# Kernel tuning notes

Hardware: AMD Instinct MI355X
Metric: run time of the kernel (lower is better)

Reference implementation:

```python
import jax, jax.numpy as jnp
import numpy as np

NT = ['SB', 'PQ', 'PV', 'NB']
SIZES = {'SB': 4000, 'PQ': 30000, 'PV': 15000, 'NB': 12000}
ETYPES = [('PV','SB'),('SB','PQ'),('SB','NB'),('PV','PQ'),('NB','PQ'),('PQ','NB'),('SB','PV'),('PQ','SB'),('NB','SB'),('PQ','PV'),('PV','NB'),('NB','PV'),('PV','PV'),('PQ','PQ'),('NB','NB')]
L, H, O, F, E, ED = 2, 128, 64, 8, 150000, 2
T = len(ETYPES)


def setup_inputs():
    key = jax.random.key(0)
    ks = iter(jax.random.split(key, 80))
    inp = {}
    for nt in NT:
        inp['x_' + nt] = jax.random.normal(next(ks), (SIZES[nt], 4), jnp.float32)
        inp['c_' + nt] = jax.random.normal(next(ks), (SIZES[nt], 4), jnp.float32)
    ei = []
    for (s, d) in ETYPES:
        ei.append(jnp.stack([jax.random.randint(next(ks), (E,), 0, SIZES[s]),
                             jax.random.randint(next(ks), (E,), 0, SIZES[d])]))
    inp['edge_index'] = jnp.stack(ei).astype(jnp.int32)  # [T, 2, E]
    inp['edge_attr'] = jax.random.normal(next(ks), (T, E, ED), jnp.float32)
    p = lambda k, *s: jax.random.normal(k, s, jnp.float32) * 0.1
    inp['Wq'] = p(next(ks), L, T, F, H); inp['bq'] = jnp.zeros((L, T, H), jnp.float32)
    inp['Wk'] = p(next(ks), L, T, F, H); inp['bk'] = jnp.zeros((L, T, H), jnp.float32)
    inp['Wv'] = p(next(ks), L, T, F, H); inp['bv'] = jnp.zeros((L, T, H), jnp.float32)
    inp['We'] = p(next(ks), L, T, ED, H); inp['be'] = jnp.zeros((L, T, H), jnp.float32)
    inp['Ws'] = p(next(ks), L, T, F, H); inp['bs'] = jnp.zeros((L, T, H), jnp.float32)
    inp['W_lin'] = p(next(ks), 2, O); inp['b_lin'] = jnp.zeros((O,), jnp.float32)
    inp['W_fc'] = p(next(ks), len(NT), O, O); inp['b_fc'] = jnp.zeros((len(NT), O), jnp.float32)
    inp['W_lin2'] = p(next(ks), 2, O); inp['b_lin2'] = jnp.zeros((O,), jnp.float32)
    return inp


def _tconv(xs, xd, src, dst, ea, Wq, bq, Wk, bk, Wv, bv, We, be, Ws, bs):
    # PyG TransformerConv, heads=1, edge_dim=2, root_weight=True, beta=False
    nd = xd.shape[0]
    q = xd @ Wq + bq            # [Nd, H]
    k = xs @ Wk + bk            # [Ns, H]
    v = xs @ Wv + bv            # [Ns, H]
    e = ea @ We + be            # [E, H]
    kj = k[src] + e
    vj = v[src] + e
    logit = (q[dst] * kj).sum(-1) / np.float32(np.sqrt(q.shape[-1]))  # [E]
    m = jax.ops.segment_max(logit, dst, num_segments=nd)
    pe = jnp.exp(logit - m[dst])
    den = jax.ops.segment_sum(pe, dst, num_segments=nd)
    alpha = pe / (den[dst] + 1e-16)  # PyG softmax epsilon
    agg = jax.ops.segment_sum(alpha[:, None] * vj, dst, num_segments=nd)
    return agg + xd @ Ws + bs   # skip connection (lin_skip)


def _group_sum(xs):
    # 'group': cat on node axis, split channels in half (P/Q), sum each half
    out = jnp.concatenate(xs, axis=0)
    half = out.shape[1] // 2
    return jnp.stack([out[:, :half].sum(1), out[:, half:].sum(1)], axis=1)  # [M, 2]


def reference(x_SB, x_PQ, x_PV, x_NB, c_SB, c_PQ, c_PV, c_NB, edge_index, edge_attr,
              Wq, bq, Wk, bk, Wv, bv, We, be, Ws, bs,
              W_lin, b_lin, W_fc, b_fc, W_lin2, b_lin2):
    xmap = {'SB': (x_SB, c_SB), 'PQ': (x_PQ, c_PQ), 'PV': (x_PV, c_PV), 'NB': (x_NB, c_NB)}
    x = {nt: jnp.concatenate(xmap[nt], axis=1) for nt in NT}  # [N, 8]
    outs = {nt: [] for nt in NT}
    for i in range(L):
        for t, (s, d) in enumerate(ETYPES):
            outs[d].append(_tconv(x[s], x[d], edge_index[t, 0], edge_index[t, 1], edge_attr[t],
                                  Wq[i, t], bq[i, t], Wk[i, t], bk[i, t], Wv[i, t], bv[i, t],
                                  We[i, t], be[i, t], Ws[i, t], bs[i, t]))
    agg = {nt: jax.nn.elu(_group_sum(outs[nt]) @ W_lin + b_lin) for nt in NT}
    # HeteroMinMaxNorm with running_min=0, running_max=1, momentum=0.1 (updated then used)
    xc = jnp.concatenate([agg[nt] for nt in NT], axis=0)
    rmin = 0.1 * xc.min()
    rmax = 0.9 + 0.1 * xc.max()
    xsc = (xc - rmin) / (rmax - rmin + 1e-5) * 2.0 - 1.0
    sizes = [agg[nt].shape[0] for nt in NT]
    splits = jnp.split(xsc, np.cumsum(sizes)[:-1].tolist(), axis=0)
    nrm = dict(zip(NT, splits))
    node_lists = {nt: [] for nt in NT}
    for i in range(L):
        for j, nt in enumerate(NT):
            node_lists[nt].append(jax.nn.elu(nrm[nt] @ W_fc[j] + b_fc[j]))
    final = [jax.nn.elu(_group_sum(node_lists[nt]) @ W_lin2 + b_lin2) for nt in NT]
    return jnp.concatenate(final, axis=0)  # [960000, 64]
```

## Files before the change

kernel.cpp:

```cpp
#include <hip/hip_runtime.h>
#include <hip/hip_fp16.h>
#include <math.h>

#define NE 150000

__constant__ int c_stype[15] = {2,0,0,2,3,1,0,1,3,1,2,3,2,1,3};
__constant__ int c_dtype[15] = {0,1,3,1,1,3,2,0,0,2,3,2,2,1,3};
__constant__ int c_slot[15]  = {0,0,0,1,2,1,0,1,2,1,2,2,3,3,3};
__constant__ int c_N[4]      = {4000,30000,15000,12000};
__constant__ int c_xoff[4]   = {0,4000,34000,49000};
__constant__ int c_cnt[4]    = {3,4,4,4};
__constant__ int c_aggoff[4] = {0,24000,264000,384000};
__constant__ int c_outoff[4] = {0,48000,528000,768000};
__constant__ int c_aggrows[4]= {24000,240000,120000,96000};
__constant__ int c_tprefix[16] = {0,4,34,46,76,106,118,133,137,141,156,168,183,198,228,240};
__constant__ int c_toff2[15] = {0,4001,34002,46003,76004,106005,118006,133007,137008,141009,156010,168011,183012,198013,228014};

typedef _Float16 f16x8 __attribute__((ext_vector_type(8)));
typedef float f32x4 __attribute__((ext_vector_type(4)));

__device__ __forceinline__ float eluf(float x){ return x > 0.0f ? x : expm1f(x); }
__device__ __forceinline__ float elufast(float x){ return x > 0.0f ? x : __expf(x)-1.0f; }
__device__ __forceinline__ unsigned encf(float f){ unsigned u=__float_as_uint(f); return (u&0x80000000u)? ~u : (u|0x80000000u); }
__device__ __forceinline__ float decf(unsigned u){ return __uint_as_float((u&0x80000000u)? (u^0x80000000u) : ~u); }
__device__ __forceinline__ float RL(float v, int l){ return __uint_as_float(__builtin_amdgcn_readlane(__float_as_uint(v), l)); }

__global__ __launch_bounds__(256) void k_build_x(
    const float* __restrict__ xSB, const float* __restrict__ cSB,
    const float* __restrict__ xPQ, const float* __restrict__ cPQ,
    const float* __restrict__ xPV, const float* __restrict__ cPV,
    const float* __restrict__ xNB, const float* __restrict__ cNB,
    float* __restrict__ xall){
  int n = blockIdx.x*256 + threadIdx.x;
  if (n >= 61000) return;
  const float *xp, *cp; int local;
  if (n < 4000)      { xp=xSB; cp=cSB; local=n; }
  else if (n < 34000){ xp=xPQ; cp=cPQ; local=n-4000; }
  else if (n < 49000){ xp=xPV; cp=cPV; local=n-34000; }
  else               { xp=xNB; cp=cNB; local=n-49000; }
  float4 a = ((const float4*)xp)[local];
  float4 b = ((const float4*)cp)[local];
  ((float4*)xall)[n*2+0] = a;
  ((float4*)xall)[n*2+1] = b;
}

__device__ __forceinline__ float dot128(const float* __restrict__ a, const float* __restrict__ b){
  const float4* a4 = (const float4*)a; const float4* b4 = (const float4*)b;
  float s = 0.f;
  #pragma unroll
  for (int h=0; h<32; h++){
    float4 A=a4[h], B=b4[h];
    s = fmaf(A.x,B.x,s); s = fmaf(A.y,B.y,s); s = fmaf(A.z,B.z,s); s = fmaf(A.w,B.w,s);
  }
  return s;
}
__device__ __forceinline__ void halfsum(const float* __restrict__ a, float& s0, float& s1){
  const float4* a4 = (const float4*)a;
  float x0=0.f, x1=0.f;
  #pragma unroll
  for (int h=0; h<16; h++){ float4 A=a4[h]; x0 += A.x+A.y+A.z+A.w; }
  #pragma unroll
  for (int h=16; h<32; h++){ float4 A=a4[h]; x1 += A.x+A.y+A.z+A.w; }
  s0=x0; s1=x1;
}

__global__ __launch_bounds__(128) void k_params(
    const float* __restrict__ Wq, const float* __restrict__ bq,
    const float* __restrict__ Wk, const float* __restrict__ bk,
    const float* __restrict__ Wv, const float* __restrict__ bv,
    const float* __restrict__ We, const float* __restrict__ be,
    const float* __restrict__ Ws, const float* __restrict__ bs,
    float* __restrict__ par){
  const int c = blockIdx.x, tid = threadIdx.x;
  const float* wq = Wq + (size_t)c*1024;
  const float* wk = Wk + (size_t)c*1024;
  const float* wv = Wv + (size_t)c*1024;
  const float* ws = Ws + (size_t)c*1024;
  const float* we = We + (size_t)c*256;
  const float* vbq = bq + (size_t)c*128;
  const float* vbk = bk + (size_t)c*128;
  const float* vbv = bv + (size_t)c*128;
  const float* vbe = be + (size_t)c*128;
  const float* vbs = bs + (size_t)c*128;
  float* P = par + (size_t)c*160;
  if (tid < 64){
    int fd = tid>>3, fs = tid&7;
    P[tid] = dot128(wq + fd*128, wk + fs*128);
    return;
  }
  const int job = tid - 64, grp = job>>3, f = job&7;
  if (grp==0) P[64+f] = dot128(wq + f*128, vbk);
  else if (grp==1) P[72+f] = dot128(wk + f*128, vbq);
  else if (grp==2) P[80+f] = dot128(wq + f*128, we);
  else if (grp==3) P[88+f] = dot128(wq + f*128, we+128);
  else if (grp==4) P[96+f] = dot128(wq + f*128, vbe);
  else if (grp==5){ float s0,s1; halfsum(wv + f*128, s0,s1); P[104+f]=s0; P[112+f]=s1; }
  else if (grp==6){ float s0,s1; halfsum(ws + f*128, s0,s1); P[120+f]=s0; P[128+f]=s1; }
  else {
    if (f==0){ P[136] = dot128(vbq, vbk);
               float a,b; halfsum(vbs, a,b); P[148]=a; P[149]=b; }
    else if (f==1) P[137] = dot128(vbq, we);
    else if (f==2) P[138] = dot128(vbq, we+128);
    else if (f==3) P[139] = dot128(vbq, vbe);
    else if (f==4){ float a=0.f,b=0.f; for(int h=0;h<64;h++){a+=we[h]; b+=we[64+h];} P[140]=a; P[141]=b; }
    else if (f==5){ float a=0.f,b=0.f; for(int h=0;h<64;h++){a+=we[128+h]; b+=we[192+h];} P[142]=a; P[143]=b; }
    else if (f==6){ float a,b; halfsum(vbv, a,b); P[144]=a; P[145]=b; }
    else          { float a,b; halfsum(vbe, a,b); P[146]=a; P[147]=b; }
  }
}

#define CHUNK 18750

__global__ __launch_bounds__(1024) void k_count(const int* __restrict__ eidx,
                                                int* __restrict__ gcnt){
  const int t = blockIdx.y;
  __shared__ int cnt[32];
  if (threadIdx.x < 32) cnt[threadIdx.x] = 0;
  __syncthreads();
  const int* __restrict__ dstp = eidx + (size_t)(t*2+1)*NE;
  const int e0 = blockIdx.x*CHUNK, e1 = min(NE, e0+CHUNK);
  for (int e=e0+threadIdx.x; e<e1; e+=1024) atomicAdd(&cnt[dstp[e]>>10], 1);
  __syncthreads();
  if (threadIdx.x < 32 && cnt[threadIdx.x] > 0)
    atomicAdd(&gcnt[c_tprefix[t] + threadIdx.x], cnt[threadIdx.x]);
}

__global__ void k_scan(const int* __restrict__ gcnt, int* __restrict__ gofs,
                       int* __restrict__ gcur){
  const int t = threadIdx.x;
  if (t >= 15) return;
  const int b0 = c_tprefix[t], b1 = c_tprefix[t+1];
  int run = t*NE;
  for (int b=b0; b<b1; b++){ gofs[b]=run; gcur[b]=run; run += gcnt[b]; }
}

__global__ __launch_bounds__(1024) void k_scatter(const int* __restrict__ eidx,
    const float* __restrict__ eattr,
    int* __restrict__ gcur, uint2* __restrict__ ebuf){
  const int t = blockIdx.y;
  __shared__ int lcnt[32], lbase[32];
  if (threadIdx.x < 32) lcnt[threadIdx.x] = 0;
  __syncthreads();
  const int* __restrict__ dstp = eidx + (size_t)(t*2+1)*NE;
  const int* __restrict__ srcp = eidx + (size_t)(t*2)*NE;
  const float2* __restrict__ ea2 = (const float2*)eattr + (size_t)t*NE;
  const int e0 = blockIdx.x*CHUNK, e1 = min(NE, e0+CHUNK);
  for (int e=e0+threadIdx.x; e<e1; e+=1024) atomicAdd(&lcnt[dstp[e]>>10], 1);
  __syncthreads();
  if (threadIdx.x < 32){
    int cchk = lcnt[threadIdx.x];
    lbase[threadIdx.x] = cchk > 0 ? atomicAdd(&gcur[c_tprefix[t]+threadIdx.x], cchk) : 0;
  }
  __syncthreads();
  if (threadIdx.x < 32) lcnt[threadIdx.x] = 0;
  __syncthreads();
  for (int e=e0+threadIdx.x; e<e1; e+=1024){
    const int d = dstp[e];
    const int tile = d>>10, dl = d&1023;
    const int pos = lbase[tile] + atomicAdd(&lcnt[tile], 1);
    const float2 ea = ea2[e];
    __half2 h2 = __floats2half2_rn(ea.x, ea.y);
    ebuf[pos] = make_uint2(((unsigned)srcp[e]<<10) | (unsigned)dl, *(unsigned*)&h2);
  }
}

__global__ __launch_bounds__(1024) void k_tsort(
    const uint2* __restrict__ ebuf,
    const int* __restrict__ gofs, const int* __restrict__ gcnt,
    uint2* __restrict__ erec, int* __restrict__ gs2, int* __restrict__ glen){
  const int b = blockIdx.x;
  int t = 0;
  while (b >= c_tprefix[t+1]) ++t;
  const int tile = b - c_tprefix[t];
  const int dt = c_dtype[t];
  const int N = c_N[dt];
  const int nbase = tile << 10;
  const int tileN = min(1024, N - nbase);
  const int tid = threadIdx.x;
  const int lane = tid & 63, wid = tid >> 6;

  __shared__ int cnt[1024];
  __shared__ int wsum[16];

  cnt[tid] = 0;
  __syncthreads();
  const int start = gofs[b], count = gcnt[b];
  for (int k=tid; k<count; k+=1024) atomicAdd(&cnt[ebuf[start+k].x & 1023u], 1);
  __syncthreads();
  const int v = cnt[tid];
  int inc = v;
  #pragma unroll
  for (int off=1; off<64; off<<=1){ int u = __shfl_up(inc, off); if (lane>=off) inc += u; }
  if (lane==63) wsum[wid] = inc;
  __syncthreads();
  if (tid==0){ int r=0; for (int k=0;k<16;k++){ int x=wsum[k]; wsum[k]=r; r+=x; } }
  __syncthreads();
  const int pref = wsum[wid] + inc - v;
  if (tid < tileN){
    gs2 [c_toff2[t] + nbase + tid] = start + pref;
    glen[c_toff2[t] + nbase + tid] = v;
  }
  cnt[tid] = pref;
  __syncthreads();

  for (int k=tid; k<count; k+=1024){
    const uint2 u2 = ebuf[start+k];
    const int dl = u2.x & 1023u;
    const int pos = start + atomicAdd(&cnt[dl], 1);
    erec[pos] = make_uint2(u2.x >> 10, u2.y);
  }
}

__global__ __launch_bounds__(256) void k_gather(
    const int* __restrict__ gs2, const int* __restrict__ glen,
    const uint2* __restrict__ erec,
    const float* __restrict__ xall, const float* __restrict__ par,
    const float* __restrict__ Wl, const float* __restrict__ bl,
    float* __restrict__ g, unsigned* __restrict__ mm){
  const int t = blockIdx.y;
  const int dt = c_dtype[t], st = c_stype[t];
  const int N = c_N[dt];
  if (blockIdx.x*256 >= N) return;
  __shared__ float sA[160], sB[160];
  __shared__ float wlb[192];
  __shared__ float smin[4], smax[4];
  const int tid = threadIdx.x;
  if (tid < 160){ sA[tid] = par[(size_t)t*160 + tid]; sB[tid] = par[(size_t)(15+t)*160 + tid]; }
  if (tid < 192) wlb[tid] = (tid<128)? Wl[tid] : bl[tid-128];
  __syncthreads();
  const int n = blockIdx.x*256 + tid;
  const bool valid = n < N;
  float lmin = 3.4e38f, lmax = -3.4e38f;
  if (valid){
    const float4* xdp = (const float4*)(xall + (size_t)(c_xoff[dt]+n)*8);
    float4 b0v = xdp[0], b1v = xdp[1];
    float xd[8] = {b0v.x,b0v.y,b0v.z,b0v.w,b1v.x,b1v.y,b1v.z,b1v.w};
    float r2a[8], r2b[8];
    #pragma unroll
    for (int fs=0; fs<8; fs++){
      float a = sA[72+fs], bb = sB[72+fs];
      #pragma unroll
      for (int fd=0; fd<8; fd++){ a = fmaf(xd[fd], sA[fd*8+fs], a); bb = fmaf(xd[fd], sB[fd*8+fs], bb); }
      r2a[fs]=a; r2b[fs]=bb;
    }
    float t0a=sA[137], t1a=sA[138], tba=sA[139], u0a=sA[136];
    float t0b=sB[137], t1b=sB[138], tbb=sB[139], u0b=sB[136];
    #pragma unroll
    for (int f=0;f<8;f++){
      t0a = fmaf(xd[f], sA[80+f], t0a);  t0b = fmaf(xd[f], sB[80+f], t0b);
      t1a = fmaf(xd[f], sA[88+f], t1a);  t1b = fmaf(xd[f], sB[88+f], t1b);
      tba = fmaf(xd[f], sA[96+f], tba);  tbb = fmaf(xd[f], sB[96+f], tbb);
      u0a = fmaf(xd[f], sA[64+f], u0a);  u0b = fmaf(xd[f], sB[64+f], u0b);
    }
    const float accda = u0a + tba, accdb = u0b + tbb;
    const int o = c_toff2[t];
    const int js = gs2[o+n], je = js + glen[o+n];
    float denA=0.f, n0A=0.f, n1A=0.f;
    float denB=0.f, n0B=0.f, n1B=0.f;
    for (int j=js; j<je; j++){
      const uint2 rec = erec[j];
      const int src = (int)rec.x;
      const __half2 h2 = *(const __half2*)&rec.y;
      const float eax = __low2float(h2), eay = __high2float(h2);
      const float4* xsp = (const float4*)(xall + (size_t)(c_xoff[st]+src)*8);
      float4 a0v = xsp[0], a1v = xsp[1];
      float xs[8] = {a0v.x,a0v.y,a0v.z,a0v.w,a1v.x,a1v.y,a1v.z,a1v.w};
      float accA = accda, accB = accdb;
      float v0A = fmaf(eax, sA[140], fmaf(eay, sA[142], sA[144]+sA[146]));
      float v1A = fmaf(eax, sA[141], fmaf(eay, sA[143], sA[145]+sA[147]));
      float v0B = fmaf(eax, sB[140], fmaf(eay, sB[142], sB[144]+sB[146]));
      float v1B = fmaf(eax, sB[141], fmaf(eay, sB[143], sB[145]+sB[147]));
      #pragma unroll
      for (int f=0;f<8;f++){
        accA = fmaf(xs[f], r2a[f], accA);   accB = fmaf(xs[f], r2b[f], accB);
        v0A  = fmaf(xs[f], sA[104+f], v0A); v0B  = fmaf(xs[f], sB[104+f], v0B);
        v1A  = fmaf(xs[f], sA[112+f], v1A); v1B  = fmaf(xs[f], sB[112+f], v1B);
      }
      accA = fmaf(eax, t0a, fmaf(eay, t1a, accA));
      accB = fmaf(eax, t0b, fmaf(eay, t1b, accB));
      const float peA = __expf(accA * 0.08838834764831845f);
      const float peB = __expf(accB * 0.08838834764831845f);
      denA += peA; n0A = fmaf(peA, v0A, n0A); n1A = fmaf(peA, v1A, n1A);
      denB += peB; n0B = fmaf(peB, v0B, n0B); n1B = fmaf(peB, v1B, n1B);
    }
    const float invA = 1.0f/(denA + 1e-16f);
    const float invB = 1.0f/(denB + 1e-16f);
    float s0a = fmaf(n0A, invA, sA[148]), s1a = fmaf(n1A, invA, sA[149]);
    float s0b = fmaf(n0B, invB, sB[148]), s1b = fmaf(n1B, invB, sB[149]);
    #pragma unroll
    for (int f=0;f<8;f++){
      s0a = fmaf(xd[f], sA[120+f], s0a); s1a = fmaf(xd[f], sA[128+f], s1a);
      s0b = fmaf(xd[f], sB[120+f], s0b); s1b = fmaf(xd[f], sB[128+f], s1b);
    }
    const int baseA = c_aggoff[dt] + (0*c_cnt[dt] + c_slot[t])*N + n;
    const int baseB = c_aggoff[dt] + (1*c_cnt[dt] + c_slot[t])*N + n;
    ((float2*)g)[baseA] = make_float2(s0a, s1a);
    ((float2*)g)[baseB] = make_float2(s0b, s1b);
    #pragma unroll
    for (int h=0;h<64;h++){
      float za = fmaf(s0a, wlb[h], fmaf(s1a, wlb[64+h], wlb[128+h]));
      float zb = fmaf(s0b, wlb[h], fmaf(s1b, wlb[64+h], wlb[128+h]));
      lmin = fminf(lmin, fminf(za,zb)); lmax = fmaxf(lmax, fmaxf(za,zb));
    }
  }
  #pragma unroll
  for (int m=32;m>=1;m>>=1){
    lmin = fminf(lmin, __shfl_xor(lmin,m));
    lmax = fmaxf(lmax, __shfl_xor(lmax,m));
  }
  const int wv = tid>>6;
  if ((tid&63)==0){ smin[wv]=lmin; smax[wv]=lmax; }
  __syncthreads();
  if (tid==0){
    float mn = fminf(fminf(smin[0],smin[1]), fminf(smin[2],smin[3]));
    float mx = fmaxf(fmaxf(smax[0],smax[1]), fmaxf(smax[2],smax[3]));
    atomicMin(&mm[0], encf(mn));
    atomicMax(&mm[1], encf(mx));
  }
}

__global__ __launch_bounds__(256, 1) void k_final(
    const float* __restrict__ g, const unsigned* __restrict__ mm,
    const float* __restrict__ Wl, const float* __restrict__ bl,
    const float* __restrict__ Wfc, const float* __restrict__ bfc,
    const float* __restrict__ Wl2, const float* __restrict__ bl2,
    float* __restrict__ out){
  const int gw = blockIdx.x*4 + (threadIdx.x>>6);
  const int l  = threadIdx.x & 63;
  const int lr = l & 15, lg = l >> 4;
  int nt, wo;
  if (gw < 375)       { nt=0; wo=0; }
  else if (gw < 4125) { nt=1; wo=375; }
  else if (gw < 6000) { nt=2; wo=4125; }
  else                { nt=3; wo=6000; }
  const int R = c_aggrows[nt];
  const int r0 = (gw - wo)*64;
  const float zmin = decf(mm[0]), zmax = decf(mm[1]);
  const float rmin = 0.1f*eluf(zmin);
  const float rmax = 0.9f + 0.1f*eluf(zmax);
  const float s2 = 2.0f/(rmax - rmin + 1e-5f);
  const float cc = fmaf(-rmin, s2, -1.0f);
  float wl0v[2][8], wl1v[2][8], blv[2][8];
  #pragma unroll
  for (int kk=0; kk<2; kk++){
    const int hb = kk*32 + lg*8;
    const float4 a0 = *(const float4*)&Wl[hb],    a1 = *(const float4*)&Wl[hb+4];
    const float4 b0 = *(const float4*)&Wl[64+hb], b1 = *(const float4*)&Wl[64+hb+4];
    const float4 c0 = *(const float4*)&bl[hb],    c1 = *(const float4*)&bl[hb+4];
    wl0v[kk][0]=a0.x; wl0v[kk][1]=a0.y; wl0v[kk][2]=a0.z; wl0v[kk][3]=a0.w;
    wl0v[kk][4]=a1.x; wl0v[kk][5]=a1.y; wl0v[kk][6]=a1.z; wl0v[kk][7]=a1.w;
    wl1v[kk][0]=b0.x; wl1v[kk][1]=b0.y; wl1v[kk][2]=b0.z; wl1v[kk][3]=b0.w;
    wl1v[kk][4]=b1.x; wl1v[kk][5]=b1.y; wl1v[kk][6]=b1.z; wl1v[kk][7]=b1.w;
    blv[kk][0]=c0.x;  blv[kk][1]=c0.y;  blv[kk][2]=c0.z;  blv[kk][3]=c0.w;
    blv[kk][4]=c1.x;  blv[kk][5]=c1.y;  blv[kk][6]=c1.z;  blv[kk][7]=c1.w;
  }
  const float* __restrict__ W = Wfc + (size_t)nt*4096;
  f16x8 bfrag[2][4];
  #pragma unroll
  for (int kk=0; kk<2; kk++){
    #pragma unroll
    for (int ntl=0; ntl<4; ntl++){
      #pragma unroll
      for (int j=0; j<8; j++){
        const int h = kk*32 + lg*8 + j;
        bfrag[kk][ntl][j] = (_Float16)W[h*64 + ntl*16 + lr];
      }
    }
  }
  const float bf0 = bfc[nt*64 + lr],      bf1 = bfc[nt*64 + 16 + lr];
  const float bf2 = bfc[nt*64 + 32 + lr], bf3 = bfc[nt*64 + 48 + lr];
  const float2* __restrict__ g2p = (const float2*)g + c_aggoff[nt] + r0;
  float ph0[4][4], ph1[4][4];
  #pragma unroll
  for (int mt=0; mt<4; mt++){
    const float2 gv = g2p[mt*16 + lr];
    f16x8 af0, af1;
    #pragma unroll
    for (int j=0; j<8; j++){
      const float z0 = fmaf(gv.x, wl0v[0][j], fmaf(gv.y, wl1v[0][j], blv[0][j]));
      const float z1 = fmaf(gv.x, wl0v[1][j], fmaf(gv.y, wl1v[1][j], blv[1][j]));
      af0[j] = (_Float16)fmaf(elufast(z0), s2, cc);
      af1[j] = (_Float16)fmaf(elufast(z1), s2, cc);
    }
    f32x4 d0 = {0.f,0.f,0.f,0.f}, d1 = {0.f,0.f,0.f,0.f};
    f32x4 d2 = {0.f,0.f,0.f,0.f}, d3 = {0.f,0.f,0.f,0.f};
    d0 = __builtin_amdgcn_mfma_f32_16x16x32_f16(af0, bfrag[0][0], d0, 0,0,0);
    d1 = __builtin_amdgcn_mfma_f32_16x16x32_f16(af0, bfrag[0][1], d1, 0,0,0);
    d2 = __builtin_amdgcn_mfma_f32_16x16x32_f16(af0, bfrag[0][2], d2, 0,0,0);
    d3 = __builtin_amdgcn_mfma_f32_16x16x32_f16(af0, bfrag[0][3], d3, 0,0,0);
    d0 = __builtin_amdgcn_mfma_f32_16x16x32_f16(af1, bfrag[1][0], d0, 0,0,0);
    d1 = __builtin_amdgcn_mfma_f32_16x16x32_f16(af1, bfrag[1][1], d1, 0,0,0);
    d2 = __builtin_amdgcn_mfma_f32_16x16x32_f16(af1, bfrag[1][2], d2, 0,0,0);
    d3 = __builtin_amdgcn_mfma_f32_16x16x32_f16(af1, bfrag[1][3], d3, 0,0,0);
    #pragma unroll
    for (int reg=0; reg<4; reg++){
      float p0 = elufast(d0[reg] + bf0) + elufast(d1[reg] + bf1);
      float p1 = elufast(d2[reg] + bf2) + elufast(d3[reg] + bf3);
      p0 += __shfl_xor(p0,1); p0 += __shfl_xor(p0,2); p0 += __shfl_xor(p0,4); p0 += __shfl_xor(p0,8);
      p1 += __shfl_xor(p1,1); p1 += __shfl_xor(p1,2); p1 += __shfl_xor(p1,4); p1 += __shfl_xor(p1,8);
      ph0[mt][reg] = p0; ph1[mt][reg] = p1;
    }
  }
  const float wl20 = Wl2[l], wl21 = Wl2[64+l], bl2v = bl2[l];
  float* __restrict__ o1 = out + ((size_t)c_outoff[nt] + r0)*64 + l;
  float* __restrict__ o2 = o1 + (size_t)R*64;
  #pragma unroll
  for (int r=0; r<64; r++){
    const int mt = r>>4, rt = r&15;
    const float h0r = RL(ph0[mt][rt&3], (rt>>2)<<4);
    const float h1r = RL(ph1[mt][rt&3], (rt>>2)<<4);
    const float f = elufast(fmaf(h0r, wl20, fmaf(h1r, wl21, bl2v)));
    o1[(size_t)r*64] = f;
    o2[(size_t)r*64] = f;
  }
}

extern "C" void kernel_launch(void* const* d_in, const int* in_sizes, int n_in,
                              void* d_out, int out_size, void* d_ws, size_t ws_size,
                              hipStream_t stream) {
  const float* xSB = (const float*)d_in[0];
  const float* cSB = (const float*)d_in[1];
  const float* xPQ = (const float*)d_in[2];
  const float* cPQ = (const float*)d_in[3];
  const float* xPV = (const float*)d_in[4];
  const float* cPV = (const float*)d_in[5];
  const float* xNB = (const float*)d_in[6];
  const float* cNB = (const float*)d_in[7];
  const int*   eidx = (const int*)d_in[8];
  const float* eattr= (const float*)d_in[9];
  const float* Wq = (const float*)d_in[10];
  const float* bq = (const float*)d_in[11];
  const float* Wk = (const float*)d_in[12];
  const float* bk = (const float*)d_in[13];
  const float* Wv = (const float*)d_in[14];
  const float* bv = (const float*)d_in[15];
  const float* We = (const float*)d_in[16];
  const float* be = (const float*)d_in[17];
  const float* Ws = (const float*)d_in[18];
  const float* bs = (const float*)d_in[19];
  const float* Wl = (const float*)d_in[20];
  const float* bl = (const float*)d_in[21];
  const float* Wfc= (const float*)d_in[22];
  const float* bfc= (const float*)d_in[23];
  const float* Wl2= (const float*)d_in[24];
  const float* bl2= (const float*)d_in[25];

  float* ws    = (float*)d_ws;
  float* xall  = ws + 0;
  float* par   = ws + 488000;
  int* gs2     = (int*)(ws + 492800);
  int* glen    = (int*)(ws + 732815);
  int* gcnt    = (int*)(ws + 972830);
  int* gofs    = (int*)(ws + 973070);
  int* gcur    = (int*)(ws + 973310);
  unsigned* mm = (unsigned*)(ws + 973550);
  uint2* ebuf  = (uint2*)(ws + 973552);
  float* g     = ws + 973552;
  uint2* erec  = (uint2*)(ws + 5473552);

  hipMemsetAsync(gcnt, 0, 240*sizeof(int), stream);
  hipMemsetAsync(mm,   0xFF, 4, stream);
  hipMemsetAsync(mm+1, 0x00, 4, stream);

  k_build_x<<<(61000+255)/256, 256, 0, stream>>>(xSB,cSB,xPQ,cPQ,xPV,cPV,xNB,cNB, xall);
  k_params<<<30, 128, 0, stream>>>(Wq,bq,Wk,bk,Wv,bv,We,be,Ws,bs, par);
  dim3 gb(8, 15);
  k_count<<<gb, 1024, 0, stream>>>(eidx, gcnt);
  k_scan<<<1, 64, 0, stream>>>(gcnt, gofs, gcur);
  k_scatter<<<gb, 1024, 0, stream>>>(eidx, eattr, gcur, ebuf);
  k_tsort<<<240, 1024, 0, stream>>>(ebuf, gofs, gcnt, erec, gs2, glen);
  dim3 gg((30000+255)/256, 15);
  k_gather<<<gg, 256, 0, stream>>>(gs2, glen, erec, xall, par, Wl, bl, g, mm);
  k_final<<<1875, 256, 0, stream>>>(g, mm, Wl, bl, Wfc, bfc, Wl2, bl2, (float*)d_out);
}
```

Before: 256.1 us.

## Fuse front-end kernels and merge tile sort with gather stage

Combines build_x, params and count into one k_front launch using block-index ranges. Fuses the per-tile counting sort with the gather/attention computation so each 1024-node tile block sorts its edges and then processes its nodes directly, removing the gs2/glen arrays and a kernel launch. k_final is restructured to emit outputs per m-tile, cutting live registers, and its occupancy hint is relaxed. Risks: the gather now runs with 1024-thread blocks and only 240 blocks, which may reduce parallelism and occupancy compared with the previous 256-thread grid.

New measurement: 273.9 us. +6.9%, slower.

```diff
diff --git a/kernel.cpp b/kernel.cpp
--- a/kernel.cpp
+++ b/kernel.cpp
@@ -14,7 +14,6 @@
 __constant__ int c_outoff[4] = {0,48000,528000,768000};
 __constant__ int c_aggrows[4]= {24000,240000,120000,96000};
 __constant__ int c_tprefix[16] = {0,4,34,46,76,106,118,133,137,141,156,168,183,198,228,240};
-__constant__ int c_toff2[15] = {0,4001,34002,46003,76004,106005,118006,133007,137008,141009,156010,168011,183012,198013,228014};
 
 typedef _Float16 f16x8 __attribute__((ext_vector_type(8)));
 typedef float f32x4 __attribute__((ext_vector_type(4)));
@@ -25,104 +24,104 @@
 __device__ __forceinline__ float decf(unsigned u){ return __uint_as_float((u&0x80000000u)? (u^0x80000000u) : ~u); }
 __device__ __forceinline__ float RL(float v, int l){ return __uint_as_float(__builtin_amdgcn_readlane(__float_as_uint(v), l)); }
 
-__global__ __launch_bounds__(256) void k_build_x(
+__device__ __forceinline__ float dot128(const float* __restrict__ a, const float* __restrict__ b){
+  const float4* a4 = (const float4*)a; const float4* b4 = (const float4*)b;
+  float s = 0.f;
+  #pragma unroll
+  for (int h=0; h<32; h++){
+    float4 A=a4[h], B=b4[h];
+    s = fmaf(A.x,B.x,s); s = fmaf(A.y,B.y,s); s = fmaf(A.z,B.z,s); s = fmaf(A.w,B.w,s);
+  }
+  return s;
+}
+__device__ __forceinline__ void halfsum(const float* __restrict__ a, float& s0, float& s1){
+  const float4* a4 = (const float4*)a;
+  float x0=0.f, x1=0.f;
+  #pragma unroll
+  for (int h=0; h<16; h++){ float4 A=a4[h]; x0 += A.x+A.y+A.z+A.w; }
+  #pragma unroll
+  for (int h=16; h<32; h++){ float4 A=a4[h]; x1 += A.x+A.y+A.z+A.w; }
+  s0=x0; s1=x1;
+}
+
+#define CHUNK 18750
+
+__global__ __launch_bounds__(1024) void k_front(
     const float* __restrict__ xSB, const float* __restrict__ cSB,
     const float* __restrict__ xPQ, const float* __restrict__ cPQ,
     const float* __restrict__ xPV, const float* __restrict__ cPV,
     const float* __restrict__ xNB, const float* __restrict__ cNB,
-    float* __restrict__ xall){
-  int n = blockIdx.x*256 + threadIdx.x;
-  if (n >= 61000) return;
-  const float *xp, *cp; int local;
-  if (n < 4000)      { xp=xSB; cp=cSB; local=n; }
-  else if (n < 34000){ xp=xPQ; cp=cPQ; local=n-4000; }
-  else if (n < 49000){ xp=xPV; cp=cPV; local=n-34000; }
-  else               { xp=xNB; cp=cNB; local=n-49000; }
-  float4 a = ((const float4*)xp)[local];
-  float4 b = ((const float4*)cp)[local];
-  ((float4*)xall)[n*2+0] = a;
-  ((float4*)xall)[n*2+1] = b;
-}
-
-__device__ __forceinline__ float dot128(const float* __restrict__ a, const float* __restrict__ b){
-  const float4* a4 = (const float4*)a; const float4* b4 = (const float4*)b;
-  float s = 0.f;
-  #pragma unroll
-  for (int h=0; h<32; h++){
-    float4 A=a4[h], B=b4[h];
-    s = fmaf(A.x,B.x,s); s = fmaf(A.y,B.y,s); s = fmaf(A.z,B.z,s); s = fmaf(A.w,B.w,s);
-  }
-  return s;
-}
-__device__ __forceinline__ void halfsum(const float* __restrict__ a, float& s0, float& s1){
-  const float4* a4 = (const float4*)a;
-  float x0=0.f, x1=0.f;
-  #pragma unroll
-  for (int h=0; h<16; h++){ float4 A=a4[h]; x0 += A.x+A.y+A.z+A.w; }
-  #pragma unroll
-  for (int h=16; h<32; h++){ float4 A=a4[h]; x1 += A.x+A.y+A.z+A.w; }
-  s0=x0; s1=x1;
-}
-
-__global__ __launch_bounds__(128) void k_params(
+    const int* __restrict__ eidx,
     const float* __restrict__ Wq, const float* __restrict__ bq,
     const float* __restrict__ Wk, const float* __restrict__ bk,
     const float* __restrict__ Wv, const float* __restrict__ bv,
     const float* __restrict__ We, const float* __restrict__ be,
     const float* __restrict__ Ws, const float* __restrict__ bs,
-    float* __restrict__ par){
-  const int c = blockIdx.x, tid = threadIdx.x;
-  const float* wq = Wq + (size_t)c*1024;
-  const float* wk = Wk + (size_t)c*1024;
-  const float* wv = Wv + (size_t)c*1024;
-  const float* ws = Ws + (size_t)c*1024;
-  const float* we = We + (size_t)c*256;
-  const float* vbq = bq + (size_t)c*128;
-  const float* vbk = bk + (size_t)c*128;
-  const float* vbv = bv + (size_t)c*128;
-  const float* vbe = be + (size_t)c*128;
-  const float* vbs = bs + (size_t)c*128;
-  float* P = par + (size_t)c*160;
-  if (tid < 64){
-    int fd = tid>>3, fs = tid&7;
-    P[tid] = dot128(wq + fd*128, wk + fs*128);
-    return;
-  }
-  const int job = tid - 64, grp = job>>3, f = job&7;
-  if (grp==0) P[64+f] = dot128(wq + f*128, vbk);
-  else if (grp==1) P[72+f] = dot128(wk + f*128, vbq);
-  else if (grp==2) P[80+f] = dot128(wq + f*128, we);
-  else if (grp==3) P[88+f] = dot128(wq + f*128, we+128);
-  else if (grp==4) P[96+f] = dot128(wq + f*128, vbe);
-  else if (grp==5){ float s0,s1; halfsum(wv + f*128, s0,s1); P[104+f]=s0; P[112+f]=s1; }
-  else if (grp==6){ float s0,s1; halfsum(ws + f*128, s0,s1); P[120+f]=s0; P[128+f]=s1; }
-  else {
-    if (f==0){ P[136] = dot128(vbq, vbk);
-               float a,b; halfsum(vbs, a,b); P[148]=a; P[149]=b; }
-    else if (f==1) P[137] = dot128(vbq, we);
-    else if (f==2) P[138] = dot128(vbq, we+128);
-    else if (f==3) P[139] = dot128(vbq, vbe);
-    else if (f==4){ float a=0.f,b=0.f; for(int h=0;h<64;h++){a+=we[h]; b+=we[64+h];} P[140]=a; P[141]=b; }
-    else if (f==5){ float a=0.f,b=0.f; for(int h=0;h<64;h++){a+=we[128+h]; b+=we[192+h];} P[142]=a; P[143]=b; }
-    else if (f==6){ float a,b; halfsum(vbv, a,b); P[144]=a; P[145]=b; }
-    else          { float a,b; halfsum(vbe, a,b); P[146]=a; P[147]=b; }
-  }
-}
-
-#define CHUNK 18750
-
-__global__ __launch_bounds__(1024) void k_count(const int* __restrict__ eidx,
-                                                int* __restrict__ gcnt){
-  const int t = blockIdx.y;
-  __shared__ int cnt[32];
-  if (threadIdx.x < 32) cnt[threadIdx.x] = 0;
-  __syncthreads();
-  const int* __restrict__ dstp = eidx + (size_t)(t*2+1)*NE;
-  const int e0 = blockIdx.x*CHUNK, e1 = min(NE, e0+CHUNK);
-  for (int e=e0+threadIdx.x; e<e1; e+=1024) atomicAdd(&cnt[dstp[e]>>10], 1);
-  __syncthreads();
-  if (threadIdx.x < 32 && cnt[threadIdx.x] > 0)
-    atomicAdd(&gcnt[c_tprefix[t] + threadIdx.x], cnt[threadIdx.x]);
+    float* __restrict__ xall, float* __restrict__ par, int* __restrict__ gcnt){
+  const int b = blockIdx.x;
+  if (b < 60){
+    const int n = b*1024 + threadIdx.x;
+    if (n >= 61000) return;
+    const float *xp, *cp; int local;
+    if (n < 4000)      { xp=xSB; cp=cSB; local=n; }
+    else if (n < 34000){ xp=xPQ; cp=cPQ; local=n-4000; }
+    else if (n < 49000){ xp=xPV; cp=cPV; local=n-34000; }
+    else               { xp=xNB; cp=cNB; local=n-49000; }
+    float4 a = ((const float4*)xp)[local];
+    float4 bb = ((const float4*)cp)[local];
+    ((float4*)xall)[n*2+0] = a;
+    ((float4*)xall)[n*2+1] = bb;
+  } else if (b < 90){
+    const int c = b - 60, tid = threadIdx.x;
+    if (tid >= 128) return;
+    const float* wq = Wq + (size_t)c*1024;
+    const float* wk = Wk + (size_t)c*1024;
+    const float* wv = Wv + (size_t)c*1024;
+    const float* ws = Ws + (size_t)c*1024;
+    const float* we = We + (size_t)c*256;
+    const float* vbq = bq + (size_t)c*128;
+    const float* vbk = bk + (size_t)c*128;
+    const float* vbv = bv + (size_t)c*128;
+    const float* vbe = be + (size_t)c*128;
+    const float* vbs = bs + (size_t)c*128;
+    float* P = par + (size_t)c*160;
+    if (tid < 64){
+      int fd = tid>>3, fs = tid&7;
+      P[tid] = dot128(wq + fd*128, wk + fs*128);
+      return;
+    }
+    const int job = tid - 64, grp = job>>3, f = job&7;
+    if (grp==0) P[64+f] = dot128(wq + f*128, vbk);
+    else if (grp==1) P[72+f] = dot128(wk + f*128, vbq);
+    else if (grp==2) P[80+f] = dot128(wq + f*128, we);
+    else if (grp==3) P[88+f] = dot128(wq + f*128, we+128);
+    else if (grp==4) P[96+f] = dot128(wq + f*128, vbe);
+    else if (grp==5){ float s0,s1; halfsum(wv + f*128, s0,s1); P[104+f]=s0; P[112+f]=s1; }
+    else if (grp==6){ float s0,s1; halfsum(ws + f*128, s0,s1); P[120+f]=s0; P[128+f]=s1; }
+    else {
+      if (f==0){ P[136] = dot128(vbq, vbk);
+                 float a,bb; halfsum(vbs, a,bb); P[148]=a; P[149]=bb; }
+      else if (f==1) P[137] = dot128(vbq, we);
+      else if (f==2) P[138] = dot128(vbq, we+128);
+      else if (f==3) P[139] = dot128(vbq, vbe);
+      else if (f==4){ float a=0.f,bb=0.f; for(int h=0;h<64;h++){a+=we[h]; bb+=we[64+h];} P[140]=a; P[141]=bb; }
+      else if (f==5){ float a=0.f,bb=0.f; for(int h=0;h<64;h++){a+=we[128+h]; bb+=we[192+h];} P[142]=a; P[143]=bb; }
+      else if (f==6){ float a,bb; halfsum(vbv, a,bb); P[144]=a; P[145]=bb; }
+      else          { float a,bb; halfsum(vbe, a,bb); P[146]=a; P[147]=bb; }
+    }
+  } else {
+    const int cb = b - 90;
+    const int t = cb / 8, chunk = cb % 8;
+    __shared__ int scnt[32];
+    if (threadIdx.x < 32) scnt[threadIdx.x] = 0;
+    __syncthreads();
+    const int* __restrict__ dstp = eidx + (size_t)(t*2+1)*NE;
+    const int e0 = chunk*CHUNK, e1 = min(NE, e0+CHUNK);
+    for (int e=e0+threadIdx.x; e<e1; e+=1024) atomicAdd(&scnt[dstp[e]>>10], 1);
+    __syncthreads();
+    if (threadIdx.x < 32 && scnt[threadIdx.x] > 0)
+      atomicAdd(&gcnt[c_tprefix[t] + threadIdx.x], scnt[threadIdx.x]);
+  }
 }
 
 __global__ void k_scan(const int* __restrict__ gcnt, int* __restrict__ gofs,
@@ -164,15 +163,18 @@
   }
 }
 
-__global__ __launch_bounds__(1024) void k_tsort(
+__global__ __launch_bounds__(1024) void k_tg(
     const uint2* __restrict__ ebuf,
     const int* __restrict__ gofs, const int* __restrict__ gcnt,
-    uint2* __restrict__ erec, int* __restrict__ gs2, int* __restrict__ glen){
+    uint2* __restrict__ erec,
+    const float* __restrict__ xall, const float* __restrict__ par,
+    const float* __restrict__ Wl, const float* __restrict__ bl,
+    float* __restrict__ g, unsigned* __restrict__ mm){
   const int b = blockIdx.x;
   int t = 0;
   while (b >= c_tprefix[t+1]) ++t;
   const int tile = b - c_tprefix[t];
-  const int dt = c_dtype[t];
+  const int dt = c_dtype[t], st = c_stype[t];
   const int N = c_N[dt];
   const int nbase = tile << 10;
   const int tileN = min(1024, N - nbase);
@@ -181,9 +183,15 @@
 
   __shared__ int cnt[1024];
   __shared__ int wsum[16];
+  __shared__ float sA[160], sB[160], wlb[192];
+  __shared__ float smin[16], smax[16];
 
   cnt[tid] = 0;
-  __syncthreads();
+  if (tid >= 512 && tid < 672){ int u=tid-512; sA[u] = par[(size_t)t*160 + u]; }
+  else if (tid >= 672 && tid < 832){ int u=tid-672; sB[u] = par[(size_t)(15+t)*160 + u]; }
+  else if (tid >= 832 && tid < 1024){ int u=tid-832; wlb[u] = (u<128)? Wl[u] : bl[u-128]; }
+  __syncthreads();
+
   const int start = gofs[b], count = gcnt[b];
   for (int k=tid; k<count; k+=1024) atomicAdd(&cnt[ebuf[start+k].x & 1023u], 1);
   __syncthreads();
@@ -196,40 +204,19 @@
   if (tid==0){ int r=0; for (int k=0;k<16;k++){ int x=wsum[k]; wsum[k]=r; r+=x; } }
   __syncthreads();
   const int pref = wsum[wid] + inc - v;
-  if (tid < tileN){
-    gs2 [c_toff2[t] + nbase + tid] = start + pref;
-    glen[c_toff2[t] + nbase + tid] = v;
-  }
+  const int js = start + pref, je = js + v;
   cnt[tid] = pref;
   __syncthreads();
-
   for (int k=tid; k<count; k+=1024){
     const uint2 u2 = ebuf[start+k];
     const int dl = u2.x & 1023u;
     const int pos = start + atomicAdd(&cnt[dl], 1);
     erec[pos] = make_uint2(u2.x >> 10, u2.y);
   }
-}
-
-__global__ __launch_bounds__(256) void k_gather(
-    const int* __restrict__ gs2, const int* __restrict__ glen,
-    const uint2* __restrict__ erec,
-    const float* __restrict__ xall, const float* __restrict__ par,
-    const float* __restrict__ Wl, const float* __restrict__ bl,
-    float* __restrict__ g, unsigned* __restrict__ mm){
-  const int t = blockIdx.y;
-  const int dt = c_dtype[t], st = c_stype[t];
-  const int N = c_N[dt];
-  if (blockIdx.x*256 >= N) return;
-  __shared__ float sA[160], sB[160];
-  __shared__ float wlb[192];
-  __shared__ float smin[4], smax[4];
-  const int tid = threadIdx.x;
-  if (tid < 160){ sA[tid] = par[(size_t)t*160 + tid]; sB[tid] = par[(size_t)(15+t)*160 + tid]; }
-  if (tid < 192) wlb[tid] = (tid<128)? Wl[tid] : bl[tid-128];
-  __syncthreads();
-  const int n = blockIdx.x*256 + tid;
-  const bool valid = n < N;
+  __syncthreads();
+
+  const bool valid = tid < tileN;
+  const int n = nbase + tid;
   float lmin = 3.4e38f, lmax = -3.4e38f;
   if (valid){
     const float4* xdp = (const float4*)(xall + (size_t)(c_xoff[dt]+n)*8);
@@ -253,8 +240,6 @@
       u0a = fmaf(xd[f], sA[64+f], u0a);  u0b = fmaf(xd[f], sB[64+f], u0b);
     }
     const float accda = u0a + tba, accdb = u0b + tbb;
-    const int o = c_toff2[t];
-    const int js = gs2[o+n], je = js + glen[o+n];
     float denA=0.f, n0A=0.f, n1A=0.f;
     float denB=0.f, n0B=0.f, n1B=0.f;
     for (int j=js; j<je; j++){
@@ -308,18 +293,17 @@
     lmin = fminf(lmin, __shfl_xor(lmin,m));
     lmax = fmaxf(lmax, __shfl_xor(lmax,m));
   }
-  const int wv = tid>>6;
-  if ((tid&63)==0){ smin[wv]=lmin; smax[wv]=lmax; }
+  if (lane==0){ smin[wid]=lmin; smax[wid]=lmax; }
   __syncthreads();
   if (tid==0){
-    float mn = fminf(fminf(smin[0],smin[1]), fminf(smin[2],smin[3]));
-    float mx = fmaxf(fmaxf(smax[0],smax[1]), fmaxf(smax[2],smax[3]));
+    float mn = smin[0], mx = smax[0];
+    for (int k=1;k<16;k++){ mn = fminf(mn, smin[k]); mx = fmaxf(mx, smax[k]); }
     atomicMin(&mm[0], encf(mn));
     atomicMax(&mm[1], encf(mx));
   }
 }
 
-__global__ __launch_bounds__(256, 1) void k_final(
+__global__ __launch_bounds__(256) void k_final(
     const float* __restrict__ g, const unsigned* __restrict__ mm,
     const float* __restrict__ Wl, const float* __restrict__ bl,
     const float* __restrict__ Wfc, const float* __restrict__ bfc,
@@ -370,7 +354,9 @@
   const float bf0 = bfc[nt*64 + lr],      bf1 = bfc[nt*64 + 16 + lr];
   const float bf2 = bfc[nt*64 + 32 + lr], bf3 = bfc[nt*64 + 48 + lr];
   const float2* __restrict__ g2p = (const float2*)g + c_aggoff[nt] + r0;
-  float ph0[4][4], ph1[4][4];
+  const float wl20 = Wl2[l], wl21 = Wl2[64+l], bl2v = bl2[l];
+  float* __restrict__ o1 = out + ((size_t)c_outoff[nt] + r0)*64 + l;
+  float* __restrict__ o2 = o1 + (size_t)R*64;
   #pragma unroll
   for (int mt=0; mt<4; mt++){
     const float2 gv = g2p[mt*16 + lr];
@@ -392,26 +378,24 @@
     d1 = __builtin_amdgcn_mfma_f32_16x16x32_f16(af1, bfrag[1][1], d1, 0,0,0);
     d2 = __builtin_amdgcn_mfma_f32_16x16x32_f16(af1, bfrag[1][2], d2, 0,0,0);
     d3 = __builtin_amdgcn_mfma_f32_16x16x32_f16(af1, bfrag[1][3], d3, 0,0,0);
+    float ph0[4], ph1[4];
     #pragma unroll
     for (int reg=0; reg<4; reg++){
       float p0 = elufast(d0[reg] + bf0) + elufast(d1[reg] + bf1);
       float p1 = elufast(d2[reg] + bf2) + elufast(d3[reg] + bf3);
       p0 += __shfl_xor(p0,1); p0 += __shfl_xor(p0,2); p0 += __shfl_xor(p0,4); p0 += __shfl_xor(p0,8);
       p1 += __shfl_xor(p1,1); p1 += __shfl_xor(p1,2); p1 += __shfl_xor(p1,4); p1 += __shfl_xor(p1,8);
-      ph0[mt][reg] = p0; ph1[mt][reg] = p1;
-    }
-  }
-  const float wl20 = Wl2[l], wl21 = Wl2[64+l], bl2v = bl2[l];
-  float* __restrict__ o1 = out + ((size_t)c_outoff[nt] + r0)*64 + l;
-  float* __restrict__ o2 = o1 + (size_t)R*64;
-  #pragma unroll
-  for (int r=0; r<64; r++){
-    const int mt = r>>4, rt = r&15;
-    const float h0r = RL(ph0[mt][rt&3], (rt>>2)<<4);
-    const float h1r = RL(ph1[mt][rt&3], (rt>>2)<<4);
-    const float f = elufast(fmaf(h0r, wl20, fmaf(h1r, wl21, bl2v)));
-    o1[(size_t)r*64] = f;
-    o2[(size_t)r*64] = f;
+      ph0[reg] = p0; ph1[reg] = p1;
+    }
+    #pragma unroll
+    for (int rt=0; rt<16; rt++){
+      const int r = mt*16 + rt;
+      const float h0r = RL(ph0[rt&3], (rt>>2)<<4);
+      const float h1r = RL(ph1[rt&3], (rt>>2)<<4);
+      const float f = elufast(fmaf(h0r, wl20, fmaf(h1r, wl21, bl2v)));
+      o1[(size_t)r*64] = f;
+      o2[(size_t)r*64] = f;
+    }
   }
 }
 
@@ -448,28 +432,24 @@
   float* ws    = (float*)d_ws;
   float* xall  = ws + 0;
   float* par   = ws + 488000;
-  int* gs2     = (int*)(ws + 492800);
-  int* glen    = (int*)(ws + 732815);
-  int* gcnt    = (int*)(ws + 972830);
-  int* gofs    = (int*)(ws + 973070);
-  int* gcur    = (int*)(ws + 973310);
-  unsigned* mm = (unsigned*)(ws + 973550);
-  uint2* ebuf  = (uint2*)(ws + 973552);
-  float* g     = ws + 973552;
-  uint2* erec  = (uint2*)(ws + 5473552);
+  int* gcnt    = (int*)(ws + 492800);
+  int* gofs    = (int*)(ws + 493040);
+  int* gcur    = (int*)(ws + 493280);
+  unsigned* mm = (unsigned*)(ws + 493520);
+  uint2* ebuf  = (uint2*)(ws + 493524);
+  uint2* erec  = (uint2*)(ws + 4993524);
+  float* g     = ws + 9493524;
 
   hipMemsetAsync(gcnt, 0, 240*sizeof(int), stream);
   hipMemsetAsync(mm,   0xFF, 4, stream);
   hipMemsetAsync(mm+1, 0x00, 4, stream);
 
-  k_build_x<<<(61000+255)/256, 256, 0, stream>>>(xSB,cSB,xPQ,cPQ,xPV,cPV,xNB,cNB, xall);
-  k_params<<<30, 128, 0, stream>>>(Wq,bq,Wk,bk,Wv,bv,We,be,Ws,bs, par);
+  k_front<<<210, 1024, 0, stream>>>(xSB,cSB,xPQ,cPQ,xPV,cPV,xNB,cNB, eidx,
+                                    Wq,bq,Wk,bk,Wv,bv,We,be,Ws,bs,
+                                    xall, par, gcnt);
+  k_scan<<<1, 64, 0, stream>>>(gcnt, gofs, gcur);
   dim3 gb(8, 15);
-  k_count<<<gb, 1024, 0, stream>>>(eidx, gcnt);
-  k_scan<<<1, 64, 0, stream>>>(gcnt, gofs, gcur);
   k_scatter<<<gb, 1024, 0, stream>>>(eidx, eattr, gcur, ebuf);
-  k_tsort<<<240, 1024, 0, stream>>>(ebuf, gofs, gcnt, erec, gs2, glen);
-  dim3 gg((30000+255)/256, 15);
-  k_gather<<<gg, 256, 0, stream>>>(gs2, glen, erec, xall, par, Wl, bl, g, mm);
+  k_tg<<<240, 1024, 0, stream>>>(ebuf, gofs, gcnt, erec, xall, par, Wl, bl, g, mm);
   k_final<<<1875, 256, 0, stream>>>(g, mm, Wl, bl, Wfc, bfc, Wl2, bl2, (float*)d_out);
 }
```
